# Kernel optimization log

Measured on AMD Instinct MI355X. Metric: run time of the kernel, lower is better.

Reference implementation:

```python
import jax, jax.numpy as jnp
import numpy as np

T = 2048        # tokens (single prefill sequence)
H = 4096        # hidden size
NQ = 32         # query heads
NKV = 8         # kv heads
HD = 128        # qk head_dim
VD = 96         # v head_dim (mismatched -> pad/slice path)
WIN = 1024      # sliding window size
E = 8           # routed experts
F = 1408        # moe intermediate
K = 2           # experts per token
EPS = 1e-6
THETA = 1e6


def setup_inputs() -> dict:
    key = jax.random.key(0)
    ks = jax.random.split(key, 10)
    s = 0.02
    return {
        "positions": jnp.arange(T, dtype=jnp.int32),
        "hidden_states": jax.random.normal(ks[0], (T, H), jnp.float32),
        "rms1_w": jnp.ones((H,), jnp.float32),
        "rms2_w": jnp.ones((H,), jnp.float32),
        "wq": jax.random.normal(ks[1], (H, NQ * HD), jnp.float32) * s,
        "wk": jax.random.normal(ks[2], (H, NKV * HD), jnp.float32) * s,
        "wv": jax.random.normal(ks[3], (H, NKV * VD), jnp.float32) * s,
        "wo": jax.random.normal(ks[4], (NQ * VD, H), jnp.float32) * s,
        "sink": jax.random.normal(ks[5], (NQ,), jnp.float32),
        "gate_w": jax.random.normal(ks[6], (H, E), jnp.float32) * s,
        "w_gate": jax.random.normal(ks[7], (E, H, F), jnp.float32) * s,
        "w_up": jax.random.normal(ks[8], (E, H, F), jnp.float32) * s,
        "w_down": jax.random.normal(ks[9], (E, F, H), jnp.float32) * s,
    }


def _rmsnorm(x, w):
    var = jnp.mean(x * x, axis=-1, keepdims=True)
    return x * jax.lax.rsqrt(var + EPS) * w


def _rope(positions, x):
    # neox style, full rotary over HD
    inv_freq = 1.0 / (THETA ** (jnp.arange(0, HD, 2, dtype=jnp.float32) / HD))
    ang = positions.astype(jnp.float32)[:, None] * inv_freq      # [T, HD/2]
    cos = jnp.cos(ang)[:, None, :]                               # [T, 1, HD/2]
    sin = jnp.sin(ang)[:, None, :]
    x1, x2 = x[..., : HD // 2], x[..., HD // 2 :]
    return jnp.concatenate([x1 * cos - x2 * sin, x2 * cos + x1 * sin], axis=-1)


def _forward(positions, hidden_states, rms1_w, rms2_w, wq, wk, wv, wo, sink,
             gate_w, w_gate, w_up, w_down):
    residual = hidden_states
    x = _rmsnorm(hidden_states, rms1_w)

    # ---- attention ----
    q = (x @ wq).reshape(T, NQ, HD)
    k = (x @ wk).reshape(T, NKV, HD)
    v = (x @ wv).reshape(T, NKV, VD)
    q = _rope(positions, q)
    k = _rope(positions, k)
    rep = NQ // NKV
    k = jnp.repeat(k, rep, axis=1)   # [T, NQ, HD]
    v = jnp.repeat(v, rep, axis=1)   # [T, NQ, VD]

    scale = HD ** -0.5
    scores = jnp.einsum('qhd,khd->hqk', q, k) * scale           # [NQ, T, T]
    i = positions[:, None]
    j = positions[None, :]
    mask = (j <= i) & ((i - j) < WIN)                            # causal + sliding window
    scores = jnp.where(mask[None, :, :], scores, jnp.float32(-1e30))
    # attention sink: extra per-head logit contributing only to the denominator
    sink_col = jnp.broadcast_to(sink[:, None, None], (NQ, T, 1))
    logits = jnp.concatenate([scores, sink_col], axis=-1)        # [NQ, T, T+1]
    probs = jax.nn.softmax(logits, axis=-1)[..., :T]
    attn = jnp.einsum('hqk,khv->qhv', probs, v)                  # [T, NQ, VD]
    attn_out = attn.reshape(T, NQ * VD) @ wo                     # [T, H]

    h = residual + attn_out

    # ---- MoE FFN ----
    x2 = _rmsnorm(h, rms2_w)
    router_logits = x2 @ gate_w                                   # [T, E]
    router_probs = jax.nn.softmax(router_logits, axis=-1)
    topk_w, topk_ids = jax.lax.top_k(router_probs, K)             # [T, K]
    topk_w = topk_w / jnp.sum(topk_w, axis=-1, keepdims=True)     # renormalize
    combine = jnp.zeros((T, E), jnp.float32).at[
        jnp.arange(T)[:, None], topk_ids].add(topk_w)             # [T, E]

    h1 = jnp.einsum('td,edf->etf', x2, w_gate)
    h2 = jnp.einsum('td,edf->etf', x2, w_up)
    eo = jnp.einsum('etf,efd->etd', jax.nn.silu(h1) * h2, w_down)  # [E, T, H]
    moe_out = jnp.einsum('etd,te->td', eo, combine)               # [T, H]

    return h + moe_out


def reference(positions, hidden_states, rms1_w, rms2_w, wq, wk, wv, wo, sink,
              gate_w, w_gate, w_up, w_down):
    return _forward(positions, hidden_states, rms1_w, rms2_w, wq, wk, wv, wo,
                    sink, gate_w, w_gate, w_up, w_down)
```

## Files before the change

kernel.cpp:

```cpp
#include <hip/hip_runtime.h>
#include <math.h>

#define T 2048
#define H 4096
#define NQ 32
#define NKV 8
#define HD 128
#define VD 96
#define WIN 1024
#define NE 8
#define FF 1408
#define TOPK 2

typedef __bf16 bf16x8 __attribute__((ext_vector_type(8)));
typedef unsigned short u16x8 __attribute__((ext_vector_type(8)));
typedef float f32x4 __attribute__((ext_vector_type(4)));
typedef unsigned short ushort_t;

__device__ __forceinline__ unsigned short f2bf(float f) {
  union { float f; unsigned u; } v; v.f = f;
  unsigned r = v.u + 0x7fffu + ((v.u >> 16) & 1u);
  return (unsigned short)(r >> 16);
}
__device__ __forceinline__ float bf2f(unsigned short h) {
  union { unsigned u; float f; } v; v.u = ((unsigned)h) << 16;
  return v.f;
}
__device__ __forceinline__ f32x4 mfma16(bf16x8 a, bf16x8 b, f32x4 c) {
  return __builtin_amdgcn_mfma_f32_16x16x32_bf16(a, b, c, 0, 0, 0);
}
__device__ __forceinline__ f32x4 fzero4() { f32x4 z = {0.f, 0.f, 0.f, 0.f}; return z; }

__device__ __forceinline__ void gl16(const void* g, void* l) {
  __builtin_amdgcn_global_load_lds(
      (const __attribute__((address_space(1))) void*)g,
      (__attribute__((address_space(3))) void*)l, 16, 0, 0);
}

template<int SPLIT, int GATHER, int EOFF, int OUTBF, int RES>
__global__ __launch_bounds__(256) void gemm_bt(
    const ushort_t* __restrict__ Ah, const ushort_t* __restrict__ Al, int lda,
    const ushort_t* __restrict__ Bh, const ushort_t* __restrict__ Bl,
    long long strideBe,
    void* __restrict__ Cp, int ldc,
    const float* __restrict__ res,
    const int* __restrict__ row_idx, const int* __restrict__ e_off,
    int M, int K)
{
  __shared__ __align__(16) ushort_t As[(SPLIT ? 2 : 1) * 4096];
  __shared__ __align__(16) ushort_t Bs[(SPLIT ? 2 : 1) * 4096];

  int bx = blockIdx.x, by = blockIdx.y;
  {
    int gx = gridDim.x, gy = gridDim.y;
    int nwg = gx * gy;
    if ((nwg & 7) == 0) {
      int id = by * gx + bx;
      int cpx = nwg >> 3;
      int id2 = (id & 7) * cpx + (id >> 3);
      bx = id2 / gy;
      by = id2 - bx * gy;
    }
  }

  int rowbase = 0, Mloc = M;
  if (EOFF) {
    int e = blockIdx.z;
    rowbase = e_off[e];
    Mloc = e_off[e + 1] - rowbase;
    Bh += strideBe * (long long)e;
    if (SPLIT) Bl += strideBe * (long long)e;
  }
  int mtile = by * 128;
  if (mtile >= Mloc) return;
  int n0 = bx * 128;

  int tid = threadIdx.x;
  int lane = tid & 63, wave = tid >> 6;
  int g = lane >> 4, cc = lane & 15;
  int wrow = (wave >> 1) * 64, wcol = (wave & 1) * 64;

  int ks = (tid & 3) << 3;
  const ushort_t *aph0, *aph1, *apl0 = nullptr, *apl1 = nullptr;
  {
    int r0 = (tid >> 2), r1 = (tid >> 2) + 64;
    long long ar0, ar1;
    if (EOFF || GATHER) {
      int g0 = mtile + r0; if (g0 >= Mloc) g0 = 0;
      int g1 = mtile + r1; if (g1 >= Mloc) g1 = 0;
      if (GATHER) { ar0 = row_idx[rowbase + g0]; ar1 = row_idx[rowbase + g1]; }
      else { ar0 = rowbase + g0; ar1 = rowbase + g1; }
    } else {
      ar0 = mtile + r0; ar1 = mtile + r1;
    }
    aph0 = Ah + ar0 * lda + ks;
    aph1 = Ah + ar1 * lda + ks;
    if (SPLIT) { apl0 = Al + ar0 * lda + ks; apl1 = Al + ar1 * lda + ks; }
  }
  const ushort_t* bph0 = Bh + (size_t)(n0 + (tid >> 2)) * K + ks;
  const ushort_t* bph1 = Bh + (size_t)(n0 + (tid >> 2) + 64) * K + ks;
  const ushort_t* bpl0 = SPLIT ? Bl + (size_t)(n0 + (tid >> 2)) * K + ks : nullptr;
  const ushort_t* bpl1 = SPLIT ? Bl + (size_t)(n0 + (tid >> 2) + 64) * K + ks : nullptr;
  ushort_t* la0 = As + tid * 8;
  ushort_t* la1 = As + (tid + 256) * 8;
  ushort_t* lb0 = Bs + tid * 8;
  ushort_t* lb1 = Bs + (tid + 256) * 8;

  f32x4 acc[4][4];
#pragma unroll
  for (int m = 0; m < 4; ++m)
#pragma unroll
    for (int n = 0; n < 4; ++n) acc[m][n] = fzero4();

  int nK = K >> 5;
  for (int kt = 0; kt < nK; ++kt) {
    int k0 = kt << 5;
    gl16(aph0 + k0, la0);
    gl16(aph1 + k0, la1);
    gl16(bph0 + k0, lb0);
    gl16(bph1 + k0, lb1);
    if (SPLIT) {
      gl16(apl0 + k0, la0 + 4096);
      gl16(apl1 + k0, la1 + 4096);
      gl16(bpl0 + k0, lb0 + 4096);
      gl16(bpl1 + k0, lb1 + 4096);
    }
    __syncthreads();
    bf16x8 avh[4], bvh[4], avl[4], bvl[4];
#pragma unroll
    for (int m = 0; m < 4; ++m) {
      int row = wrow + m * 16 + cc;
      avh[m] = *(const bf16x8*)&As[row * 32 + g * 8];
      if (SPLIT) avl[m] = *(const bf16x8*)&As[4096 + row * 32 + g * 8];
    }
#pragma unroll
    for (int n = 0; n < 4; ++n) {
      int row = wcol + n * 16 + cc;
      bvh[n] = *(const bf16x8*)&Bs[row * 32 + g * 8];
      if (SPLIT) bvl[n] = *(const bf16x8*)&Bs[4096 + row * 32 + g * 8];
    }
#pragma unroll
    for (int m = 0; m < 4; ++m)
#pragma unroll
      for (int n = 0; n < 4; ++n) {
        acc[m][n] = mfma16(avh[m], bvh[n], acc[m][n]);
        if (SPLIT) {
          acc[m][n] = mfma16(avh[m], bvl[n], acc[m][n]);
          acc[m][n] = mfma16(avl[m], bvh[n], acc[m][n]);
        }
      }
    __syncthreads();
  }

#pragma unroll
  for (int m = 0; m < 4; ++m) {
    int rl = wrow + m * 16 + g * 4;
#pragma unroll
    for (int n = 0; n < 4; ++n) {
      int col = n0 + wcol + n * 16 + cc;
#pragma unroll
      for (int r = 0; r < 4; ++r) {
        int grow = mtile + rl + r;
        if (grow < Mloc) {
          size_t off = (size_t)(rowbase + grow) * ldc + col;
          float vv = acc[m][n][r];
          if (OUTBF) {
            ((ushort_t*)Cp)[off] = f2bf(vv);
          } else {
            if (RES) vv += res[off];
            ((float*)Cp)[off] = vv;
          }
        }
      }
    }
  }
}

template<int SPLITOUT>
__global__ __launch_bounds__(256) void tconv_kernel(
    const float* __restrict__ src, int ldsrc,
    ushort_t* __restrict__ dh, ushort_t* __restrict__ dl,
    int lddst, int dro, long long sE, long long dE)
{
  __shared__ float tile[64][65];
  int e = blockIdx.z;
  src += sE * (long long)e;
  dh += dE * (long long)e;
  if (SPLITOUT) dl += dE * (long long)e;
  int c0 = blockIdx.x * 64;
  int r0 = blockIdx.y * 64;
  int tid = threadIdx.x;
#pragma unroll
  for (int i = 0; i < 4; ++i) {
    int idx = tid + i * 256;
    int r = idx >> 4, c4 = (idx & 15) << 2;
    float4 v = *(const float4*)&src[(size_t)(r0 + r) * ldsrc + c0 + c4];
    tile[r][c4 + 0] = v.x; tile[r][c4 + 1] = v.y;
    tile[r][c4 + 2] = v.z; tile[r][c4 + 3] = v.w;
  }
  __syncthreads();
#pragma unroll
  for (int i = 0; i < 2; ++i) {
    int idx = tid + i * 256;
    int c = idx >> 3, r8 = (idx & 7) << 3;
    u16x8 hv, lv;
#pragma unroll
    for (int j = 0; j < 8; ++j) {
      float f = tile[r8 + j][c];
      unsigned short hh = f2bf(f);
      hv[j] = hh;
      if (SPLITOUT) lv[j] = f2bf(f - bf2f(hh));
    }
    size_t o = (size_t)(dro + c0 + c) * lddst + r0 + r8;
    *(u16x8*)&dh[o] = hv;
    if (SPLITOUT) *(u16x8*)&dl[o] = lv;
  }
}

__global__ __launch_bounds__(256) void rmsnorm_hl_kernel(const float* __restrict__ in,
    const float* __restrict__ w, ushort_t* __restrict__ oh, ushort_t* __restrict__ ol)
{
  int t = blockIdx.x;
  int tid = threadIdx.x;
  const float4* rp = (const float4*)(in + (size_t)t * H);
  const float4* wp = (const float4*)w;
  float4 vv[4];
  float ss = 0.f;
#pragma unroll
  for (int i = 0; i < 4; ++i) {
    vv[i] = rp[tid + i * 256];
    ss += vv[i].x * vv[i].x + vv[i].y * vv[i].y + vv[i].z * vv[i].z + vv[i].w * vv[i].w;
  }
#pragma unroll
  for (int off = 32; off > 0; off >>= 1) ss += __shfl_xor(ss, off);
  __shared__ float red[4];
  if ((tid & 63) == 0) red[tid >> 6] = ss;
  __syncthreads();
  float tot = red[0] + red[1] + red[2] + red[3];
  float rs = rsqrtf(tot * (1.f / H) + 1e-6f);
#pragma unroll
  for (int i = 0; i < 4; ++i) {
    float4 x = vv[i];
    float4 ww = wp[tid + i * 256];
    float y0 = x.x * rs * ww.x, y1 = x.y * rs * ww.y;
    float y2 = x.z * rs * ww.z, y3 = x.w * rs * ww.w;
    ushort4 hh, ll;
    hh.x = f2bf(y0); hh.y = f2bf(y1); hh.z = f2bf(y2); hh.w = f2bf(y3);
    ll.x = f2bf(y0 - bf2f(hh.x)); ll.y = f2bf(y1 - bf2f(hh.y));
    ll.z = f2bf(y2 - bf2f(hh.z)); ll.w = f2bf(y3 - bf2f(hh.w));
    *(ushort4*)&oh[(size_t)t * H + (tid + i * 256) * 4] = hh;
    *(ushort4*)&ol[(size_t)t * H + (tid + i * 256) * 4] = ll;
  }
}

__global__ __launch_bounds__(256) void rmsnorm_fh_kernel(const float* __restrict__ in,
    const float* __restrict__ w, float* __restrict__ of, ushort_t* __restrict__ oh)
{
  int t = blockIdx.x;
  int tid = threadIdx.x;
  const float4* rp = (const float4*)(in + (size_t)t * H);
  const float4* wp = (const float4*)w;
  float4 vv[4];
  float ss = 0.f;
#pragma unroll
  for (int i = 0; i < 4; ++i) {
    vv[i] = rp[tid + i * 256];
    ss += vv[i].x * vv[i].x + vv[i].y * vv[i].y + vv[i].z * vv[i].z + vv[i].w * vv[i].w;
  }
#pragma unroll
  for (int off = 32; off > 0; off >>= 1) ss += __shfl_xor(ss, off);
  __shared__ float red[4];
  if ((tid & 63) == 0) red[tid >> 6] = ss;
  __syncthreads();
  float tot = red[0] + red[1] + red[2] + red[3];
  float rs = rsqrtf(tot * (1.f / H) + 1e-6f);
#pragma unroll
  for (int i = 0; i < 4; ++i) {
    float4 x = vv[i];
    float4 ww = wp[tid + i * 256];
    float4 o;
    o.x = x.x * rs * ww.x; o.y = x.y * rs * ww.y;
    o.z = x.z * rs * ww.z; o.w = x.w * rs * ww.w;
    *(float4*)&of[(size_t)t * H + (tid + i * 256) * 4] = o;
    ushort4 hh;
    hh.x = f2bf(o.x); hh.y = f2bf(o.y); hh.z = f2bf(o.z); hh.w = f2bf(o.w);
    *(ushort4*)&oh[(size_t)t * H + (tid + i * 256) * 4] = hh;
  }
}

__global__ __launch_bounds__(256) void rope_pack_kernel(const int* __restrict__ pos,
    const float* __restrict__ qkv,
    ushort_t* __restrict__ qh, ushort_t* __restrict__ ql,
    ushort_t* __restrict__ kh, ushort_t* __restrict__ kl,
    ushort_t* __restrict__ vh, ushort_t* __restrict__ vl)
{
  int t = blockIdx.x;
  float p = (float)pos[t];
  int tid = threadIdx.x;
  const float* row = qkv + (size_t)t * 5888;
  for (int idx = tid; idx < (NQ + NKV) * 64; idx += 256) {
    int col; ushort_t *dh, *dl; size_t dbase; int d;
    if (idx < NQ * 64) {
      int hh = idx >> 6; d = idx & 63;
      col = hh * HD + d;
      dbase = (size_t)t * (NQ * HD) + hh * HD;
      dh = qh; dl = ql;
    } else {
      int j = idx - NQ * 64;
      int hh = j >> 6; d = j & 63;
      col = 4096 + hh * HD + d;
      dbase = (size_t)t * (NKV * HD) + hh * HD;
      dh = kh; dl = kl;
    }
    float inv = exp2f(-19.931568569324174f * (float)(2 * d) * (1.0f / 128.0f));
    float ang = p * inv;
    float sn = sinf(ang), cs = cosf(ang);
    float x1 = row[col], x2 = row[col + 64];
    float o1 = x1 * cs - x2 * sn;
    float o2 = x2 * cs + x1 * sn;
    unsigned short h1 = f2bf(o1), h2 = f2bf(o2);
    dh[dbase + d] = h1; dl[dbase + d] = f2bf(o1 - bf2f(h1));
    dh[dbase + d + 64] = h2; dl[dbase + d + 64] = f2bf(o2 - bf2f(h2));
  }
  for (int idx = tid; idx < NKV * VD; idx += 256) {
    float v = row[5120 + idx];
    size_t o = (size_t)t * (NKV * VD) + idx;
    unsigned short hh = f2bf(v);
    vh[o] = hh; vl[o] = f2bf(v - bf2f(hh));
  }
}

__global__ __launch_bounds__(256) void attn_kernel(
    const ushort_t* __restrict__ qh, const ushort_t* __restrict__ ql,
    const ushort_t* __restrict__ kh, const ushort_t* __restrict__ kl,
    const ushort_t* __restrict__ vhp, const ushort_t* __restrict__ vlp,
    const float* __restrict__ sink, const int* __restrict__ pos,
    ushort_t* __restrict__ aoh, ushort_t* __restrict__ aol)
{
  __shared__ __align__(16) ushort_t Qs[2][64][136];
  __shared__ __align__(16) ushort_t Ks[2][32][136];
  __shared__ __align__(16) ushort_t Vt[2][96][40];
  __shared__ __align__(16) ushort_t Ps[2][4][16][40];
  __shared__ int posq[64];
  __shared__ int posk[32];

  const float SCALE = 0.08838834764831843f;
  int qtile = blockIdx.x, head = blockIdx.y;
  {
    int id = head * 32 + qtile;
    int id2 = (id & 7) * 128 + (id >> 3);
    head = id2 >> 5;
    qtile = id2 & 31;
  }
  int qs = qtile * 64;
  int kvh = head >> 2;
  int tid = threadIdx.x;
  int lane = tid & 63, wave = tid >> 6;
  int g = lane >> 4, cc = lane & 15;
  int wq0 = wave * 16;

#pragma unroll
  for (int i = 0; i < 4; ++i) {
    int c = tid + i * 256;
    int row = c >> 4, ks = (c & 15) << 3;
    size_t gofs = (size_t)(qs + row) * (NQ * HD) + head * HD + ks;
    *(u16x8*)&Qs[0][row][ks] = *(const u16x8*)(qh + gofs);
    *(u16x8*)&Qs[1][row][ks] = *(const u16x8*)(ql + gofs);
  }
  if (tid < 64) posq[tid] = pos[qs + tid];

  float m_r[4], l_r[4];
  f32x4 acc_o[6];
#pragma unroll
  for (int r = 0; r < 4; ++r) { m_r[r] = -__builtin_huge_valf(); l_r[r] = 0.f; }
#pragma unroll
  for (int n = 0; n < 6; ++n) acc_o[n] = fzero4();

  int kstart = qs - (WIN - 1);
  if (kstart < 0) kstart = 0;
  kstart &= ~31;
  int kend = qs + 63;

  for (int k0 = kstart; k0 <= kend; k0 += 32) {
    __syncthreads();
#pragma unroll
    for (int i = 0; i < 2; ++i) {
      int c = tid + i * 256;
      int row = c >> 4, ks = (c & 15) << 3;
      size_t gofs = (size_t)(k0 + row) * (NKV * HD) + kvh * HD + ks;
      *(u16x8*)&Ks[0][row][ks] = *(const u16x8*)(kh + gofs);
      *(u16x8*)&Ks[1][row][ks] = *(const u16x8*)(kl + gofs);
    }
#pragma unroll
    for (int i = 0; i < 3; ++i) {
      int qd = tid + i * 256;
      int key = qd / 24, vq = qd % 24;
      size_t gofs = (size_t)(k0 + key) * (NKV * VD) + kvh * VD + vq * 4;
      ushort4 a = *(const ushort4*)(vhp + gofs);
      ushort4 b = *(const ushort4*)(vlp + gofs);
      Vt[0][vq * 4 + 0][key] = a.x; Vt[0][vq * 4 + 1][key] = a.y;
      Vt[0][vq * 4 + 2][key] = a.z; Vt[0][vq * 4 + 3][key] = a.w;
      Vt[1][vq * 4 + 0][key] = b.x; Vt[1][vq * 4 + 1][key] = b.y;
      Vt[1][vq * 4 + 2][key] = b.z; Vt[1][vq * 4 + 3][key] = b.w;
    }
    if (tid < 32) posk[tid] = pos[k0 + tid];
    __syncthreads();

    bf16x8 aqh[4], aql[4];
#pragma unroll
    for (int kk = 0; kk < 4; ++kk) {
      aqh[kk] = *(const bf16x8*)&Qs[0][wq0 + cc][kk * 32 + g * 8];
      aql[kk] = *(const bf16x8*)&Qs[1][wq0 + cc][kk * 32 + g * 8];
    }
    f32x4 sacc[2];
    sacc[0] = fzero4(); sacc[1] = fzero4();
#pragma unroll
    for (int kb = 0; kb < 2; ++kb)
#pragma unroll
      for (int kk = 0; kk < 4; ++kk) {
        bf16x8 bh = *(const bf16x8*)&Ks[0][kb * 16 + cc][kk * 32 + g * 8];
        bf16x8 bl = *(const bf16x8*)&Ks[1][kb * 16 + cc][kk * 32 + g * 8];
        sacc[kb] = mfma16(aqh[kk], bh, sacc[kb]);
        sacc[kb] = mfma16(aqh[kk], bl, sacc[kb]);
        sacc[kb] = mfma16(aql[kk], bh, sacc[kb]);
      }

    int j0 = posk[cc], j1 = posk[16 + cc];
#pragma unroll
    for (int r = 0; r < 4; ++r) {
      int irow = posq[wq0 + g * 4 + r];
      float s0 = sacc[0][r] * SCALE;
      float s1 = sacc[1][r] * SCALE;
      bool ok0 = (j0 <= irow) && (irow - j0 < WIN);
      bool ok1 = (j1 <= irow) && (irow - j1 < WIN);
      if (!ok0) s0 = -1e30f;
      if (!ok1) s1 = -1e30f;
      float rm = fmaxf(s0, s1);
#pragma unroll
      for (int off = 1; off < 16; off <<= 1) rm = fmaxf(rm, __shfl_xor(rm, off));
      float mn = fmaxf(m_r[r], rm);
      float p0 = ok0 ? __expf(s0 - mn) : 0.f;
      float p1 = ok1 ? __expf(s1 - mn) : 0.f;
      float rs = p0 + p1;
#pragma unroll
      for (int off = 1; off < 16; off <<= 1) rs += __shfl_xor(rs, off);
      float alpha = __expf(m_r[r] - mn);
      l_r[r] = l_r[r] * alpha + rs;
      m_r[r] = mn;
#pragma unroll
      for (int n = 0; n < 6; ++n) acc_o[n][r] *= alpha;
      unsigned short p0h = f2bf(p0), p1h = f2bf(p1);
      Ps[0][wave][g * 4 + r][cc] = p0h;
      Ps[1][wave][g * 4 + r][cc] = f2bf(p0 - bf2f(p0h));
      Ps[0][wave][g * 4 + r][16 + cc] = p1h;
      Ps[1][wave][g * 4 + r][16 + cc] = f2bf(p1 - bf2f(p1h));
    }
    bf16x8 pah = *(const bf16x8*)&Ps[0][wave][cc][g * 8];
    bf16x8 pal = *(const bf16x8*)&Ps[1][wave][cc][g * 8];
#pragma unroll
    for (int n = 0; n < 6; ++n) {
      bf16x8 bh = *(const bf16x8*)&Vt[0][n * 16 + cc][g * 8];
      bf16x8 bl = *(const bf16x8*)&Vt[1][n * 16 + cc][g * 8];
      acc_o[n] = mfma16(pah, bh, acc_o[n]);
      acc_o[n] = mfma16(pah, bl, acc_o[n]);
      acc_o[n] = mfma16(pal, bh, acc_o[n]);
    }
  }

  float snk = sink[head];
#pragma unroll
  for (int r = 0; r < 4; ++r) {
    float m2 = fmaxf(m_r[r], snk);
    float alpha = __expf(m_r[r] - m2);
    float denom = l_r[r] * alpha + __expf(snk - m2);
    float inv = 1.f / denom;
    int row = qs + wq0 + g * 4 + r;
#pragma unroll
    for (int n = 0; n < 6; ++n) {
      float val = acc_o[n][r] * alpha * inv;
      size_t off = (size_t)row * (NQ * VD) + head * VD + n * 16 + cc;
      unsigned short hh = f2bf(val);
      aoh[off] = hh;
      aol[off] = f2bf(val - bf2f(hh));
    }
  }
}

__global__ __launch_bounds__(64) void router_kernel(const float* __restrict__ x2,
    const float* __restrict__ gw, float* __restrict__ topkw, int* __restrict__ topkid)
{
  int t = blockIdx.x;
  int lane = threadIdx.x;
  float acc[NE];
#pragma unroll
  for (int e = 0; e < NE; ++e) acc[e] = 0.f;
  for (int hh = lane; hh < H; hh += 64) {
    float xv = x2[(size_t)t * H + hh];
    const float* g = gw + (size_t)hh * NE;
#pragma unroll
    for (int e = 0; e < NE; ++e) acc[e] = fmaf(xv, g[e], acc[e]);
  }
#pragma unroll
  for (int e = 0; e < NE; ++e)
#pragma unroll
    for (int off = 32; off > 0; off >>= 1) acc[e] += __shfl_xor(acc[e], off);
  if (lane == 0) {
    int b1 = 0; float v1 = acc[0];
#pragma unroll
    for (int e = 1; e < NE; ++e) { if (acc[e] > v1) { v1 = acc[e]; b1 = e; } }
    int b2 = -1; float v2 = -3.4e38f;
#pragma unroll
    for (int e = 0; e < NE; ++e) { if (e != b1 && acc[e] > v2) { v2 = acc[e]; b2 = e; } }
    float e2 = __expf(v2 - v1);
    float s = 1.f + e2;
    topkw[t * 2] = 1.f / s;
    topkw[t * 2 + 1] = e2 / s;
    topkid[t * 2] = b1;
    topkid[t * 2 + 1] = b2;
  }
}

__global__ __launch_bounds__(256) void route_build_kernel(
    const int* __restrict__ topkid, int* __restrict__ idssort,
    int* __restrict__ prow, int* __restrict__ eoffs)
{
  __shared__ int cnt[NE];
  __shared__ int off[NE + 1];
  __shared__ int cur[NE];
  int tid = threadIdx.x;
  if (tid < NE) cnt[tid] = 0;
  __syncthreads();
  for (int p = tid; p < T * TOPK; p += 256) atomicAdd(&cnt[topkid[p]], 1);
  __syncthreads();
  if (tid == 0) {
    off[0] = 0;
    for (int e = 0; e < NE; ++e) off[e + 1] = off[e] + cnt[e];
  }
  __syncthreads();
  if (tid < NE) cur[tid] = off[tid];
  __syncthreads();
  for (int p = tid; p < T * TOPK; p += 256) {
    int e = topkid[p];
    int ppos = atomicAdd(&cur[e], 1);
    idssort[ppos] = p >> 1;
    prow[p] = ppos;
  }
  if (tid <= NE) eoffs[tid] = off[tid];
}

__global__ __launch_bounds__(256) void silu_mul_kernel(
    const ushort_t* __restrict__ h12, ushort_t* __restrict__ oh)
{
  int id = blockIdx.x * 256 + threadIdx.x;
  int r = id / 176;
  int c8 = (id % 176) * 8;
  u16x8 a = *(const u16x8*)&h12[(size_t)r * 2816 + c8];
  u16x8 b = *(const u16x8*)&h12[(size_t)r * 2816 + 1408 + c8];
  u16x8 o;
#pragma unroll
  for (int j = 0; j < 8; ++j) {
    float x = bf2f(a[j]), y = bf2f(b[j]);
    float rr = x / (1.f + __expf(-x)) * y;
    o[j] = f2bf(rr);
  }
  *(u16x8*)&oh[(size_t)r * 1408 + c8] = o;
}

__global__ __launch_bounds__(256) void combine_kernel(const float* __restrict__ h,
    const float* __restrict__ eo, const float* __restrict__ topkw,
    const int* __restrict__ prow, float* __restrict__ out)
{
  int t = blockIdx.x, tid = threadIdx.x;
  float w0 = topkw[t * 2], w1 = topkw[t * 2 + 1];
  const float4* e0 = (const float4*)(eo + (size_t)prow[t * 2] * H);
  const float4* e1 = (const float4*)(eo + (size_t)prow[t * 2 + 1] * H);
  const float4* hp = (const float4*)(h + (size_t)t * H);
  float4* op = (float4*)(out + (size_t)t * H);
#pragma unroll
  for (int i = 0; i < 4; ++i) {
    int idx = tid + i * 256;
    float4 a = hp[idx], b = e0[idx], c = e1[idx];
    float4 o;
    o.x = a.x + w0 * b.x + w1 * c.x;
    o.y = a.y + w0 * b.y + w1 * c.y;
    o.z = a.z + w0 * b.z + w1 * c.z;
    o.w = a.w + w0 * b.w + w1 * c.w;
    op[idx] = o;
  }
}

extern "C" void kernel_launch(void* const* d_in, const int* in_sizes, int n_in,
                              void* d_out, int out_size, void* d_ws, size_t ws_size,
                              hipStream_t stream) {
  const int*   pos   = (const int*)d_in[0];
  const float* hid   = (const float*)d_in[1];
  const float* rms1w = (const float*)d_in[2];
  const float* rms2w = (const float*)d_in[3];
  const float* wq    = (const float*)d_in[4];
  const float* wk    = (const float*)d_in[5];
  const float* wv    = (const float*)d_in[6];
  const float* wo    = (const float*)d_in[7];
  const float* sink  = (const float*)d_in[8];
  const float* gw    = (const float*)d_in[9];
  const float* wgate = (const float*)d_in[10];
  const float* wup   = (const float*)d_in[11];
  const float* wdown = (const float*)d_in[12];
  float* out = (float*)d_out;

  const size_t MB = 1048576ull;
  if (ws_size < 462ull * MB) return;

  char* ws = (char*)d_ws;
  ushort_t* wqkvT_h = (ushort_t*)(ws + 0 * MB);
  ushort_t* wqkvT_l = (ushort_t*)(ws + 47 * MB);
  ushort_t* woT_h   = (ushort_t*)(ws + 94 * MB);
  ushort_t* woT_l   = (ushort_t*)(ws + 118 * MB);
  ushort_t* wgupT   = (ushort_t*)(ws + 0 * MB);
  ushort_t* wdownT  = (ushort_t*)(ws + 176 * MB);
  char* A0 = ws + 264 * MB;
  ushort_t* x1h = (ushort_t*)(A0 + 0 * MB);
  ushort_t* x1l = (ushort_t*)(A0 + 16 * MB);
  ushort_t* kh  = (ushort_t*)(A0 + 32 * MB);
  ushort_t* kl  = (ushort_t*)(A0 + 36 * MB);
  ushort_t* vh  = (ushort_t*)(A0 + 40 * MB);
  ushort_t* vl  = (ushort_t*)(A0 + 43 * MB);
  ushort_t* aoh = (ushort_t*)(A0 + 46 * MB);
  ushort_t* aol = (ushort_t*)(A0 + 58 * MB);
  ushort_t* qh  = (ushort_t*)(A0 + 0 * MB);
  ushort_t* ql  = (ushort_t*)(A0 + 16 * MB);
  float* eo   = (float*)(A0 + 0 * MB);
  float* qkvf = (float*)(A0 + 70 * MB);
  ushort_t* h12b = (ushort_t*)(A0 + 70 * MB);
  ushort_t* h1h  = (ushort_t*)(A0 + 93 * MB);
  float* h   = (float*)(A0 + 116 * MB);
  float* x2  = (float*)(A0 + 148 * MB);
  ushort_t* x2h = (ushort_t*)(A0 + 180 * MB);
  char* sm = A0 + 196 * MB;
  float* topkw  = (float*)(sm);
  int*  topkid  = (int*)(sm + 16384);
  int*  prow    = (int*)(sm + 32768);
  int*  idssort = (int*)(sm + 49152);
  int*  eoffs   = (int*)(sm + 65536);

  tconv_kernel<1><<<dim3(64, 64, 1), 256, 0, stream>>>(wq, 4096, wqkvT_h, wqkvT_l, 4096, 0, 0, 0);
  tconv_kernel<1><<<dim3(16, 64, 1), 256, 0, stream>>>(wk, 1024, wqkvT_h, wqkvT_l, 4096, 4096, 0, 0);
  tconv_kernel<1><<<dim3(12, 64, 1), 256, 0, stream>>>(wv, 768, wqkvT_h, wqkvT_l, 4096, 5120, 0, 0);
  tconv_kernel<1><<<dim3(64, 48, 1), 256, 0, stream>>>(wo, 4096, woT_h, woT_l, 3072, 0, 0, 0);
  tconv_kernel<0><<<dim3(64, 22, 8), 256, 0, stream>>>(wdown, 4096, wdownT, nullptr,
      1408, 0, 1408LL * 4096, 4096LL * 1408);

  rmsnorm_hl_kernel<<<T, 256, 0, stream>>>(hid, rms1w, x1h, x1l);

  gemm_bt<1, 0, 0, 0, 0><<<dim3(46, 16, 1), 256, 0, stream>>>(
      x1h, x1l, H, wqkvT_h, wqkvT_l, 0, qkvf, 5888, nullptr, nullptr, nullptr, T, H);

  rope_pack_kernel<<<T, 256, 0, stream>>>(pos, qkvf, qh, ql, kh, kl, vh, vl);

  attn_kernel<<<dim3(T / 64, NQ, 1), 256, 0, stream>>>(qh, ql, kh, kl, vh, vl,
      sink, pos, aoh, aol);

  gemm_bt<1, 0, 0, 0, 1><<<dim3(32, 16, 1), 256, 0, stream>>>(
      aoh, aol, NQ * VD, woT_h, woT_l, 0, h, H, hid, nullptr, nullptr, T, NQ * VD);

  rmsnorm_fh_kernel<<<T, 256, 0, stream>>>(h, rms2w, x2, x2h);

  router_kernel<<<T, 64, 0, stream>>>(x2, gw, topkw, topkid);
  route_build_kernel<<<1, 256, 0, stream>>>(topkid, idssort, prow, eoffs);

  tconv_kernel<0><<<dim3(22, 64, 8), 256, 0, stream>>>(wgate, 1408, wgupT, nullptr, 4096, 0,
      4096LL * 1408, 2816LL * 4096);
  tconv_kernel<0><<<dim3(22, 64, 8), 256, 0, stream>>>(wup, 1408, wgupT, nullptr, 4096, 1408,
      4096LL * 1408, 2816LL * 4096);
  gemm_bt<0, 1, 1, 1, 0><<<dim3(22, 32, 8), 256, 0, stream>>>(
      x2h, nullptr, H, wgupT, nullptr, 2816LL * 4096, h12b, 2816, nullptr, idssort, eoffs, 0, H);
  silu_mul_kernel<<<2816, 256, 0, stream>>>(h12b, h1h);
  gemm_bt<0, 0, 1, 0, 0><<<dim3(32, 32, 8), 256, 0, stream>>>(
      h1h, nullptr, FF, wdownT, nullptr, 4096LL * 1408, eo, H, nullptr, nullptr, eoffs, 0, FF);

  combine_kernel<<<T, 256, 0, stream>>>(h, eo, topkw, prow, out);
}
```

Before: 1.480 ms.

## Pre-transpose V in a separate kernel and keep Q fragments in registers

Adds a kernel that writes V as transposed bf16 hi/lo planes ([kvh][vd][t]). The attention kernel can then fill its V^T shared tile with 16-byte vector copies instead of scattered 2-byte shared-memory writes. Q fragments now load straight from global memory into registers once, before the key loop, instead of being staged through shared memory and re-read on every iteration. This cuts shared-memory traffic and footprint in the attention loop, at the cost of one extra small kernel launch.

```diff
diff --git a/kernel.cpp b/kernel.cpp
--- a/kernel.cpp
+++ b/kernel.cpp
@@ -217,6 +217,36 @@
   }
 }
 
+__global__ __launch_bounds__(256) void vtrans_kernel(const float* __restrict__ qkv,
+    ushort_t* __restrict__ vth, ushort_t* __restrict__ vtl)
+{
+  __shared__ float tile[32][33];
+  int t0 = blockIdx.x * 32;
+  int vd0 = blockIdx.y * 32;
+  int kvh = blockIdx.z;
+  int tid = threadIdx.x;
+  {
+    int tr = tid >> 3, c4 = (tid & 7) << 2;
+    float4 v = *(const float4*)&qkv[(size_t)(t0 + tr) * 5888 + 5120 + kvh * VD + vd0 + c4];
+    tile[tr][c4 + 0] = v.x; tile[tr][c4 + 1] = v.y;
+    tile[tr][c4 + 2] = v.z; tile[tr][c4 + 3] = v.w;
+  }
+  __syncthreads();
+  {
+    int vd = tid >> 3, t4 = (tid & 7) << 2;
+    ushort4 hh, ll;
+    float f0 = tile[t4 + 0][vd], f1 = tile[t4 + 1][vd];
+    float f2 = tile[t4 + 2][vd], f3 = tile[t4 + 3][vd];
+    hh.x = f2bf(f0); ll.x = f2bf(f0 - bf2f(hh.x));
+    hh.y = f2bf(f1); ll.y = f2bf(f1 - bf2f(hh.y));
+    hh.z = f2bf(f2); ll.z = f2bf(f2 - bf2f(hh.z));
+    hh.w = f2bf(f3); ll.w = f2bf(f3 - bf2f(hh.w));
+    size_t o = (size_t)kvh * (VD * T) + (size_t)(vd0 + vd) * T + t0 + t4;
+    *(ushort4*)&vth[o] = hh;
+    *(ushort4*)&vtl[o] = ll;
+  }
+}
+
 __global__ __launch_bounds__(256) void rmsnorm_hl_kernel(const float* __restrict__ in,
     const float* __restrict__ w, ushort_t* __restrict__ oh, ushort_t* __restrict__ ol)
 {
@@ -291,8 +321,7 @@
 __global__ __launch_bounds__(256) void rope_pack_kernel(const int* __restrict__ pos,
     const float* __restrict__ qkv,
     ushort_t* __restrict__ qh, ushort_t* __restrict__ ql,
-    ushort_t* __restrict__ kh, ushort_t* __restrict__ kl,
-    ushort_t* __restrict__ vh, ushort_t* __restrict__ vl)
+    ushort_t* __restrict__ kh, ushort_t* __restrict__ kl)
 {
   int t = blockIdx.x;
   float p = (float)pos[t];
@@ -322,22 +351,15 @@
     dh[dbase + d] = h1; dl[dbase + d] = f2bf(o1 - bf2f(h1));
     dh[dbase + d + 64] = h2; dl[dbase + d + 64] = f2bf(o2 - bf2f(h2));
   }
-  for (int idx = tid; idx < NKV * VD; idx += 256) {
-    float v = row[5120 + idx];
-    size_t o = (size_t)t * (NKV * VD) + idx;
-    unsigned short hh = f2bf(v);
-    vh[o] = hh; vl[o] = f2bf(v - bf2f(hh));
-  }
 }
 
 __global__ __launch_bounds__(256) void attn_kernel(
     const ushort_t* __restrict__ qh, const ushort_t* __restrict__ ql,
     const ushort_t* __restrict__ kh, const ushort_t* __restrict__ kl,
-    const ushort_t* __restrict__ vhp, const ushort_t* __restrict__ vlp,
+    const ushort_t* __restrict__ vth, const ushort_t* __restrict__ vtl,
     const float* __restrict__ sink, const int* __restrict__ pos,
     ushort_t* __restrict__ aoh, ushort_t* __restrict__ aol)
 {
-  __shared__ __align__(16) ushort_t Qs[2][64][136];
   __shared__ __align__(16) ushort_t Ks[2][32][136];
   __shared__ __align__(16) ushort_t Vt[2][96][40];
   __shared__ __align__(16) ushort_t Ps[2][4][16][40];
@@ -358,14 +380,16 @@
   int lane = tid & 63, wave = tid >> 6;
   int g = lane >> 4, cc = lane & 15;
   int wq0 = wave * 16;
-
-#pragma unroll
-  for (int i = 0; i < 4; ++i) {
-    int c = tid + i * 256;
-    int row = c >> 4, ks = (c & 15) << 3;
-    size_t gofs = (size_t)(qs + row) * (NQ * HD) + head * HD + ks;
-    *(u16x8*)&Qs[0][row][ks] = *(const u16x8*)(qh + gofs);
-    *(u16x8*)&Qs[1][row][ks] = *(const u16x8*)(ql + gofs);
+  size_t vbase = (size_t)kvh * (VD * T);
+
+  bf16x8 aqh[4], aql[4];
+  {
+    size_t qoff = (size_t)(qs + wq0 + cc) * (NQ * HD) + head * HD + g * 8;
+#pragma unroll
+    for (int kk = 0; kk < 4; ++kk) {
+      aqh[kk] = *(const bf16x8*)(qh + qoff + kk * 32);
+      aql[kk] = *(const bf16x8*)(ql + qoff + kk * 32);
+    }
   }
   if (tid < 64) posq[tid] = pos[qs + tid];
 
@@ -393,25 +417,17 @@
     }
 #pragma unroll
     for (int i = 0; i < 3; ++i) {
-      int qd = tid + i * 256;
-      int key = qd / 24, vq = qd % 24;
-      size_t gofs = (size_t)(k0 + key) * (NKV * VD) + kvh * VD + vq * 4;
-      ushort4 a = *(const ushort4*)(vhp + gofs);
-      ushort4 b = *(const ushort4*)(vlp + gofs);
-      Vt[0][vq * 4 + 0][key] = a.x; Vt[0][vq * 4 + 1][key] = a.y;
-      Vt[0][vq * 4 + 2][key] = a.z; Vt[0][vq * 4 + 3][key] = a.w;
-      Vt[1][vq * 4 + 0][key] = b.x; Vt[1][vq * 4 + 1][key] = b.y;
-      Vt[1][vq * 4 + 2][key] = b.z; Vt[1][vq * 4 + 3][key] = b.w;
+      int id = tid + i * 256;
+      int plane = id >> 9;
+      plane = (id >= 384) ? 1 : 0;
+      int r = id - plane * 384;
+      int vd = r >> 2, kc = (r & 3) << 3;
+      const ushort_t* src = (plane ? vtl : vth) + vbase + (size_t)vd * T + k0 + kc;
+      *(u16x8*)&Vt[plane][vd][kc] = *(const u16x8*)src;
     }
     if (tid < 32) posk[tid] = pos[k0 + tid];
     __syncthreads();
 
-    bf16x8 aqh[4], aql[4];
-#pragma unroll
-    for (int kk = 0; kk < 4; ++kk) {
-      aqh[kk] = *(const bf16x8*)&Qs[0][wq0 + cc][kk * 32 + g * 8];
-      aql[kk] = *(const bf16x8*)&Qs[1][wq0 + cc][kk * 32 + g * 8];
-    }
     f32x4 sacc[2];
     sacc[0] = fzero4(); sacc[1] = fzero4();
 #pragma unroll
@@ -622,8 +638,8 @@
   ushort_t* x1l = (ushort_t*)(A0 + 16 * MB);
   ushort_t* kh  = (ushort_t*)(A0 + 32 * MB);
   ushort_t* kl  = (ushort_t*)(A0 + 36 * MB);
-  ushort_t* vh  = (ushort_t*)(A0 + 40 * MB);
-  ushort_t* vl  = (ushort_t*)(A0 + 43 * MB);
+  ushort_t* vtTh = (ushort_t*)(A0 + 40 * MB);
+  ushort_t* vtTl = (ushort_t*)(A0 + 43 * MB);
   ushort_t* aoh = (ushort_t*)(A0 + 46 * MB);
   ushort_t* aol = (ushort_t*)(A0 + 58 * MB);
   ushort_t* qh  = (ushort_t*)(A0 + 0 * MB);
@@ -654,9 +670,10 @@
   gemm_bt<1, 0, 0, 0, 0><<<dim3(46, 16, 1), 256, 0, stream>>>(
       x1h, x1l, H, wqkvT_h, wqkvT_l, 0, qkvf, 5888, nullptr, nullptr, nullptr, T, H);
 
-  rope_pack_kernel<<<T, 256, 0, stream>>>(pos, qkvf, qh, ql, kh, kl, vh, vl);
-
-  attn_kernel<<<dim3(T / 64, NQ, 1), 256, 0, stream>>>(qh, ql, kh, kl, vh, vl,
+  rope_pack_kernel<<<T, 256, 0, stream>>>(pos, qkvf, qh, ql, kh, kl);
+  vtrans_kernel<<<dim3(64, 3, 8), 256, 0, stream>>>(qkvf, vtTh, vtTl);
+
+  attn_kernel<<<dim3(T / 64, NQ, 1), 256, 0, stream>>>(qh, ql, kh, kl, vtTh, vtTl,
       sink, pos, aoh, aol);
 
   gemm_bt<1, 0, 0, 0, 1><<<dim3(32, 16, 1), 256, 0, stream>>>(
```

New measurement: 1.357 ms. 1.09x faster.
